# Optimization experiments

Hardware: AMD Instinct MI355X
Metric: run time of the kernel (lower is better)

## Reference

```python
import jax, jax.numpy as jnp
import numpy as np

B, S, D, H = 2, 2048, 1024, 16
DK = D // H

def setup_inputs() -> dict:
    key = jax.random.key(0)
    ks = jax.random.split(key, 12)
    sc = 0.02
    return {
        "q": jax.random.normal(ks[0], (B, S, D), jnp.float32),
        "k": jax.random.normal(ks[1], (B, S, D), jnp.float32),
        "v": jax.random.normal(ks[2], (B, S, D), jnp.float32),
        "mask": jnp.ones((1, 1, S, S), jnp.int32),
        "w_q": jax.random.normal(ks[3], (D, D), jnp.float32) * sc,
        "b_q": jnp.zeros((D,), jnp.float32),
        "w_k": jax.random.normal(ks[4], (D, D), jnp.float32) * sc,
        "b_k": jnp.zeros((D,), jnp.float32),
        "w_v": jax.random.normal(ks[5], (D, D), jnp.float32) * sc,
        "b_v": jnp.zeros((D,), jnp.float32),
        "w_o": jax.random.normal(ks[6], (D, D), jnp.float32) * sc,
        "b_o": jnp.zeros((D,), jnp.float32),
    }

def reference(q, k, v, mask, w_q, b_q, w_k, b_k, w_v, b_v, w_o, b_o):
    # torch Linear: y = x @ W.T + b, W is [out, in]
    def lin(x, w, b):
        return jnp.einsum('bsd,ed->bse', x, w) + b
    # project and split heads -> [B, H, S, DK]
    def heads(x):
        return x.reshape(B, S, H, DK).transpose(0, 2, 1, 3)
    Q = heads(lin(q, w_q, b_q))
    K = heads(lin(k, w_k, b_k))
    V = heads(lin(v, w_v, b_v))
    scores = jnp.einsum('bhqd,bhkd->bhqk', Q, K) / jnp.sqrt(jnp.float32(DK))
    scores = jnp.where(mask == 0, jnp.float32(-1e9), scores)
    attn = jax.nn.softmax(scores, axis=-1)  # dropout p=0 -> identity
    ctx = jnp.einsum('bhqk,bhkd->bhqd', attn, V)
    ctx = ctx.transpose(0, 2, 1, 3).reshape(B, S, D)
    return lin(ctx, w_o, b_o)
```

## Files before the change

### kernel.cpp

```cpp
#include <hip/hip_runtime.h>
#include <stdint.h>


#define S_LEN 2048
#define LOG2E 1.4426950408889634f

using bf16x8 = __attribute__((ext_vector_type(8))) __bf16;
using f32x4 = __attribute__((ext_vector_type(4))) float;
using f32x16 = __attribute__((ext_vector_type(16))) float;
using u32x4 = __attribute__((ext_vector_type(4))) unsigned int;

__device__ __forceinline__ unsigned short f2bf(float x) {
  unsigned int u = __builtin_bit_cast(unsigned int, x);
  u += 0x7fffu + ((u >> 16) & 1u);
  return (unsigned short)(u >> 16);
}

__device__ __forceinline__ void gload_lds16(const void* g, void* l) {
  __builtin_amdgcn_global_load_lds(
      (const __attribute__((address_space(1))) void*)g,
      (__attribute__((address_space(3))) void*)l, 16, 0, 0);
}

__device__ __forceinline__ unsigned int cvtpk(float lo, float hi) {
  unsigned int r;
  asm("v_cvt_pk_bf16_f32 %0, %1, %2" : "=v"(r) : "v"(lo), "v"(hi));
  return r;
}

__device__ __forceinline__ bf16x8 mkfrag(float p0, float p1, float p2, float p3,
                                         float p4, float p5, float p6, float p7) {
  auto r02 = __builtin_amdgcn_permlane32_swap(cvtpk(p0, p1), cvtpk(p4, p5),
                                              false, false);
  auto r13 = __builtin_amdgcn_permlane32_swap(cvtpk(p2, p3), cvtpk(p6, p7),
                                              false, false);
  u32x4 w = {(unsigned int)r02[0], (unsigned int)r13[0], (unsigned int)r02[1],
             (unsigned int)r13[1]};
  return __builtin_bit_cast(bf16x8, w);
}

__global__ void cvt4_kernel(const float* __restrict__ s0,
                            const float* __restrict__ s1,
                            const float* __restrict__ s2,
                            const float* __restrict__ s3,
                            unsigned short* __restrict__ d0,
                            unsigned short* __restrict__ d1,
                            unsigned short* __restrict__ d2,
                            unsigned short* __restrict__ d3, int n4) {
  const int which = blockIdx.y;
  const float* src = which == 0 ? s0 : which == 1 ? s1 : which == 2 ? s2 : s3;
  unsigned short* dst = which == 0 ? d0 : which == 1 ? d1 : which == 2 ? d2 : d3;
  int i = blockIdx.x * blockDim.x + threadIdx.x;
  int stride = gridDim.x * blockDim.x;
  for (; i < n4; i += stride) {
    float4 v = ((const float4*)src)[i];
    ushort4 o;
    o.x = f2bf(v.x);
    o.y = f2bf(v.y);
    o.z = f2bf(v.z);
    o.w = f2bf(v.w);
    ((ushort4*)dst)[i] = o;
  }
}

template <int OMODE>
__device__ __forceinline__ void qkv64_body(
    unsigned short* As, unsigned short* Bs, const float* __restrict__ X,
    const unsigned short* __restrict__ W, const float* __restrict__ bias,
    unsigned short* __restrict__ dst, float scale, int tx, int ty) {
  const int tid = threadIdx.x;
  const int wid = tid >> 6, lane = tid & 63;
  const int l15 = lane & 15, lg = lane >> 4;
  const int bm = ty * 64, bn = tx * 128;
  const int wr = (wid >> 1) * 32, wc = (wid & 1) * 64;

  const f32x4 fz = {0.f, 0.f, 0.f, 0.f};
  f32x4 acc[2][4];
#pragma unroll
  for (int m = 0; m < 2; ++m)
#pragma unroll
    for (int n = 0; n < 4; ++n) acc[m][n] = fz;

  const int ar = tid >> 2;
  const float* Af = X + (size_t)(bm + ar) * 1024 + (tid & 3) * 8;
  const int sA = (tid & 3) ^ ((tid >> 3) & 3);
  const int srow = lane >> 2;
  const int scolz = ((lane & 3) ^ ((lane >> 3) & 3)) * 8;
  const int rcol = (lg ^ ((l15 >> 1) & 3)) * 8;

  for (int kt = 0; kt < 1024; kt += 32) {
    float4 a0 = *(const float4*)(Af + kt);
    float4 a1 = *(const float4*)(Af + kt + 4);
#pragma unroll
    for (int c = 0; c < 2; ++c) {
      int ch = wid * 2 + c;
      gload_lds16(W + (size_t)(bn + ch * 16 + srow) * 1024 + kt + scolz,
                  Bs + ch * 512);
    }
    u32x4 p = {cvtpk(a0.x, a0.y), cvtpk(a0.z, a0.w), cvtpk(a1.x, a1.y),
               cvtpk(a1.z, a1.w)};
    *(u32x4*)&As[ar * 32 + sA * 8] = p;
    __syncthreads();

    bf16x8 af[2], bf[4];
#pragma unroll
    for (int m = 0; m < 2; ++m)
      af[m] = *(const bf16x8*)&As[(wr + m * 16 + l15) * 32 + rcol];
#pragma unroll
    for (int n = 0; n < 4; ++n)
      bf[n] = *(const bf16x8*)&Bs[(wc + n * 16 + l15) * 32 + rcol];

#pragma unroll
    for (int m = 0; m < 2; ++m)
#pragma unroll
      for (int n = 0; n < 4; ++n) {
        if (OMODE == 2)
          acc[m][n] = __builtin_amdgcn_mfma_f32_16x16x32_bf16(bf[n], af[m],
                                                              acc[m][n], 0, 0, 0);
        else
          acc[m][n] = __builtin_amdgcn_mfma_f32_16x16x32_bf16(af[m], bf[n],
                                                              acc[m][n], 0, 0, 0);
      }
    __syncthreads();
  }

#pragma unroll
  for (int m = 0; m < 2; ++m)
#pragma unroll
    for (int n = 0; n < 4; ++n)
#pragma unroll
      for (int j = 0; j < 4; ++j) {
        float a = acc[m][n][j];
        if (OMODE == 2) {
          int gn = bn + wc + n * 16 + lg * 4 + j;
          int gm = bm + wr + m * 16 + l15;
          float v = a + bias[gn];
          int b = gm >> 11, s = gm & 2047;
          int h = gn >> 6, dk = gn & 63;
          dst[(((size_t)(b * 16 + h)) * 64 + dk) * 2048 + s] = f2bf(v);
        } else {
          int gm = bm + wr + m * 16 + lg * 4 + j;
          int gn = bn + wc + n * 16 + l15;
          float v = (a + bias[gn]) * scale;
          int b = gm >> 11, s = gm & 2047;
          int h = gn >> 6, dk = gn & 63;
          dst[(((size_t)(b * 16 + h)) * 2048 + s) * 64 + dk] = f2bf(v);
        }
      }
}

__global__ __launch_bounds__(256) void gemm_qkv(
    const float* __restrict__ X0, const float* __restrict__ X1,
    const float* __restrict__ X2, const unsigned short* __restrict__ W0,
    const unsigned short* __restrict__ W1,
    const unsigned short* __restrict__ W2, const float* __restrict__ b0,
    const float* __restrict__ b1, const float* __restrict__ b2,
    unsigned short* __restrict__ dq, unsigned short* __restrict__ dk,
    unsigned short* __restrict__ dv) {
  __shared__ unsigned short As[64 * 32];
  __shared__ unsigned short Bs[128 * 32];
  const int lin = blockIdx.x + 8 * (blockIdx.y + 64 * blockIdx.z);
  const int xcd = lin & 7, v = lin >> 3;
  const int panel = xcd * 24 + (v >> 3);
  const int tx = v & 7;
  const int z = panel >> 6, ty = panel & 63;
  if (z == 0)
    qkv64_body<0>(As, Bs, X0, W0, b0, dq, 0.125f * LOG2E, tx, ty);
  else if (z == 1)
    qkv64_body<0>(As, Bs, X1, W1, b1, dk, 1.0f, tx, ty);
  else
    qkv64_body<2>(As, Bs, X2, W2, b2, dv, 1.0f, tx, ty);
}

__global__ __launch_bounds__(256) void gemm_out(
    const unsigned short* __restrict__ X, const unsigned short* __restrict__ W,
    const float* __restrict__ bias, float* __restrict__ dstF) {
  const int lin = blockIdx.x + 8 * blockIdx.y;
  const int xcd = lin & 7, v = lin >> 3;
  const int ty = xcd * 8 + (v >> 3);
  const int tx = v & 7;

  __shared__ unsigned short As[3][64 * 32];
  __shared__ unsigned short Bs[3][128 * 32];
  const int tid = threadIdx.x;
  const int wid = tid >> 6, lane = tid & 63;
  const int l15 = lane & 15, lg = lane >> 4;
  const int bm = ty * 64, bn = tx * 128;
  const int wr = (wid >> 1) * 32, wc = (wid & 1) * 64;

  const f32x4 fz = {0.f, 0.f, 0.f, 0.f};
  f32x4 acc[2][4];
#pragma unroll
  for (int m = 0; m < 2; ++m)
#pragma unroll
    for (int n = 0; n < 4; ++n) acc[m][n] = fz;

  const int srow = lane >> 2;
  const int scolz = ((lane & 3) ^ ((lane >> 3) & 3)) * 8;
  const int rcol = (lg ^ ((l15 >> 1) & 3)) * 8;

#define GSTAGE(buf, kt)                                                       \
  {                                                                           \
    gload_lds16(X + (size_t)(bm + wid * 16 + srow) * 1024 + (kt) + scolz,     \
                &As[buf][wid * 512]);                                         \
    _Pragma("unroll") for (int c = 0; c < 2; ++c) {                           \
      int ch = wid * 2 + c;                                                   \
      gload_lds16(W + (size_t)(bn + ch * 16 + srow) * 1024 + (kt) + scolz,    \
                  &Bs[buf][ch * 512]);                                        \
    }                                                                         \
  }

  GSTAGE(0, 0)
  GSTAGE(1, 32)
  int cur = 0;

  for (int it = 0; it < 32; ++it) {
    if (it < 31) {
      asm volatile("s_waitcnt vmcnt(3)\n\ts_barrier" ::: "memory");
    } else {
      asm volatile("s_waitcnt vmcnt(0)\n\ts_barrier" ::: "memory");
    }
    if (it < 30) {
      int nb = cur >= 1 ? cur - 1 : cur + 2;
      GSTAGE(nb, (it + 2) * 32)
    }

    bf16x8 af[2], bf[4];
#pragma unroll
    for (int m = 0; m < 2; ++m)
      af[m] = *(const bf16x8*)&As[cur][(wr + m * 16 + l15) * 32 + rcol];
#pragma unroll
    for (int n = 0; n < 4; ++n)
      bf[n] = *(const bf16x8*)&Bs[cur][(wc + n * 16 + l15) * 32 + rcol];

#pragma unroll
    for (int m = 0; m < 2; ++m)
#pragma unroll
      for (int n = 0; n < 4; ++n)
        acc[m][n] = __builtin_amdgcn_mfma_f32_16x16x32_bf16(af[m], bf[n],
                                                            acc[m][n], 0, 0, 0);
    cur = cur == 2 ? 0 : cur + 1;
  }
#undef GSTAGE

#pragma unroll
  for (int m = 0; m < 2; ++m)
#pragma unroll
    for (int n = 0; n < 4; ++n)
#pragma unroll
      for (int j = 0; j < 4; ++j) {
        int gm = bm + wr + m * 16 + lg * 4 + j;
        int gn = bn + wc + n * 16 + l15;
        dstF[(size_t)gm * 1024 + gn] = acc[m][n][j] + bias[gn];
      }
}

__global__ __launch_bounds__(256) void attn_kernel(
    const unsigned short* __restrict__ Q,
    const unsigned short* __restrict__ K,
    const unsigned short* __restrict__ VT,
    unsigned short* __restrict__ CTX) {
  const int orig = blockIdx.x;
  const int wg = (orig & 7) * 64 + (orig >> 3);
  const int bh = wg >> 4;
  const int qb = wg & 15;
  const int tid = threadIdx.x;
  const int w = tid >> 6;
  const int lane = tid & 63;
  const int l31 = lane & 31;
  const int hi = lane >> 5;
  const int q0 = qb * 128 + w * 32;

  __shared__ __align__(16) unsigned short Ks[3][64][64];
  __shared__ __align__(16) unsigned short Vs[3][64][64];
  __shared__ float ls[4][32];

  const unsigned short* Qg = Q + ((size_t)bh * S_LEN + q0) * 64;
  const unsigned short* Kg = K + (size_t)bh * S_LEN * 64;
  const unsigned short* Vg = VT + (size_t)bh * 64 * S_LEN;

  bf16x8 qf[4];
#pragma unroll
  for (int kc = 0; kc < 4; ++kc)
    qf[kc] = *(const bf16x8*)&Qg[l31 * 64 + kc * 16 + hi * 8];

  const int srow = lane >> 3;
  const int sslot = (lane & 7) ^ srow;

#define STAGE(buf, kt)                                                         \
  {                                                                            \
    gload_lds16(Kg + ((size_t)((kt) + w * 16 + srow)) * 64 + sslot * 8,        \
                &Ks[buf][w * 16][0]);                                          \
    gload_lds16(Kg + ((size_t)((kt) + w * 16 + 8 + srow)) * 64 + sslot * 8,    \
                &Ks[buf][w * 16 + 8][0]);                                      \
    gload_lds16(Vg + ((size_t)(w * 16 + srow)) * S_LEN + (kt) + sslot * 8,     \
                &Vs[buf][w * 16][0]);                                          \
    gload_lds16(Vg + ((size_t)(w * 16 + 8 + srow)) * S_LEN + (kt) + sslot * 8, \
                &Vs[buf][w * 16 + 8][0]);                                      \
  }

  f32x16 O0 = {}, O1 = {};
  float m = -1e30f, lsum = 0.f;

  STAGE(0, 0)
  STAGE(1, 64)
  int cur = 0;

  for (int t = 0; t < 32; ++t) {
    if (t < 31) {
      asm volatile("s_waitcnt vmcnt(4)\n\ts_barrier" ::: "memory");
    } else {
      asm volatile("s_waitcnt vmcnt(0)\n\ts_barrier" ::: "memory");
    }
    if (t < 30) {
      int nb = cur >= 1 ? cur - 1 : cur + 2;
      STAGE(nb, (t + 2) * 64)
    }

    f32x16 s0 = {}, s1 = {};
    __builtin_amdgcn_s_setprio(1);
#pragma unroll
    for (int kc = 0; kc < 4; ++kc) {
      const int col = ((kc * 2 + hi) ^ (l31 & 7)) * 8;
      bf16x8 kf0 = *(const bf16x8*)&Ks[cur][l31][col];
      bf16x8 kf1 = *(const bf16x8*)&Ks[cur][32 + l31][col];
      s0 = __builtin_amdgcn_mfma_f32_32x32x16_bf16(kf0, qf[kc], s0, 0, 0, 0);
      s1 = __builtin_amdgcn_mfma_f32_32x32x16_bf16(kf1, qf[kc], s1, 0, 0, 0);
    }
    __builtin_amdgcn_s_setprio(0);

    float tmax[8];
#pragma unroll
    for (int i = 0; i < 8; ++i)
      tmax[i] = fmaxf(fmaxf(s0[i], s0[i + 8]), fmaxf(s1[i], s1[i + 8]));
    float pm = fmaxf(fmaxf(fmaxf(tmax[0], tmax[1]), fmaxf(tmax[2], tmax[3])),
                     fmaxf(fmaxf(tmax[4], tmax[5]), fmaxf(tmax[6], tmax[7])));
    pm = fmaxf(pm, __shfl_xor(pm, 32, 64));

    if (!__all(pm - m <= 8.0f)) {
      float mn = fmaxf(m, pm);
      float al = exp2f(m - mn);
      m = mn;
      lsum *= al;
      ls[w][l31] = al;
#pragma unroll
      for (int r = 0; r < 16; ++r) {
        float a = ls[w][(r & 3) + 8 * (r >> 2) + 4 * hi];
        O0[r] *= a;
        O1[r] *= a;
      }
    }

#pragma unroll
    for (int r = 0; r < 16; ++r) {
      s0[r] = exp2f(s0[r] - m);
      s1[r] = exp2f(s1[r] - m);
    }
    float sa = 0.f, sb = 0.f, sc = 0.f, sd = 0.f;
#pragma unroll
    for (int r = 0; r < 4; ++r) {
      sa += s0[r];
      sb += s0[r + 4];
      sc += s0[r + 8];
      sd += s0[r + 12];
      sa += s1[r];
      sb += s1[r + 4];
      sc += s1[r + 8];
      sd += s1[r + 12];
    }
    float ts = (sa + sb) + (sc + sd);
    ts += __shfl_xor(ts, 32, 64);
    lsum += ts;

    bf16x8 pa0 = mkfrag(s0[0], s0[1], s0[2], s0[3], s0[4], s0[5], s0[6], s0[7]);
    bf16x8 pa1 =
        mkfrag(s0[8], s0[9], s0[10], s0[11], s0[12], s0[13], s0[14], s0[15]);
    bf16x8 pa2 = mkfrag(s1[0], s1[1], s1[2], s1[3], s1[4], s1[5], s1[6], s1[7]);
    bf16x8 pa3 =
        mkfrag(s1[8], s1[9], s1[10], s1[11], s1[12], s1[13], s1[14], s1[15]);

    __builtin_amdgcn_s_setprio(1);
#pragma unroll
    for (int kc = 0; kc < 4; ++kc) {
      const int col = ((kc * 2 + hi) ^ (l31 & 7)) * 8;
      bf16x8 v0 = *(const bf16x8*)&Vs[cur][l31][col];
      bf16x8 v1 = *(const bf16x8*)&Vs[cur][32 + l31][col];
      bf16x8 pa = (kc == 0) ? pa0 : (kc == 1) ? pa1 : (kc == 2) ? pa2 : pa3;
      O0 = __builtin_amdgcn_mfma_f32_32x32x16_bf16(pa, v0, O0, 0, 0, 0);
      O1 = __builtin_amdgcn_mfma_f32_32x32x16_bf16(pa, v1, O1, 0, 0, 0);
    }
    __builtin_amdgcn_s_setprio(0);

    cur = cur == 2 ? 0 : cur + 1;
  }

  ls[w][l31] = lsum;
  const int b = bh >> 4, h = bh & 15;
#pragma unroll
  for (int r = 0; r < 16; ++r) {
    int qr = (r & 3) + 8 * (r >> 2) + 4 * hi;
    float inv = __builtin_amdgcn_rcpf(ls[w][qr]);
    size_t base = ((size_t)b * S_LEN + q0 + qr) * 1024 + h * 64;
    CTX[base + l31] = f2bf(O0[r] * inv);
    CTX[base + 32 + l31] = f2bf(O1[r] * inv);
  }
#undef STAGE
}

extern "C" void kernel_launch(void* const* d_in, const int* in_sizes, int n_in,
                              void* d_out, int out_size, void* d_ws,
                              size_t ws_size, hipStream_t stream) {
  const float* q = (const float*)d_in[0];
  const float* k = (const float*)d_in[1];
  const float* v = (const float*)d_in[2];
  const float* wq = (const float*)d_in[4];
  const float* bq = (const float*)d_in[5];
  const float* wk = (const float*)d_in[6];
  const float* bk = (const float*)d_in[7];
  const float* wv = (const float*)d_in[8];
  const float* bv = (const float*)d_in[9];
  const float* wo = (const float*)d_in[10];
  const float* bo = (const float*)d_in[11];
  float* out = (float*)d_out;

  const size_t NTOK = 4096 * 1024;
  unsigned short* ws = (unsigned short*)d_ws;
  unsigned short* wqb = ws;
  unsigned short* wkb = wqb + 1048576;
  unsigned short* wvb = wkb + 1048576;
  unsigned short* wob = wvb + 1048576;
  unsigned short* Qp = wob + 1048576;
  unsigned short* Kp = Qp + NTOK;
  unsigned short* Vt = Kp + NTOK;
  unsigned short* CTX = Vt + NTOK;

  cvt4_kernel<<<dim3(256, 4), 256, 0, stream>>>(wq, wk, wv, wo, wqb, wkb, wvb,
                                                wob, 262144);

  gemm_qkv<<<dim3(8, 64, 3), 256, 0, stream>>>(q, k, v, wqb, wkb, wvb, bq, bk,
                                               bv, Qp, Kp, Vt);

  attn_kernel<<<512, 256, 0, stream>>>(Qp, Kp, Vt, CTX);

  gemm_out<<<dim3(8, 64), 256, 0, stream>>>(CTX, wob, bo, out);
}
```

Before: 149.4 us.

## Pre-convert activations, pipeline QKV GEMM, split attention KV into two halves

Measured after the change: 159.7 us. 1.07x slower.

```diff
diff --git a/kernel.cpp b/kernel.cpp
--- a/kernel.cpp
+++ b/kernel.cpp
@@ -14,6 +14,11 @@
   unsigned int u = __builtin_bit_cast(unsigned int, x);
   u += 0x7fffu + ((u >> 16) & 1u);
   return (unsigned short)(u >> 16);
+}
+
+__device__ __forceinline__ float bf2f(unsigned short u) {
+  unsigned int x = ((unsigned int)u) << 16;
+  return __builtin_bit_cast(float, x);
 }
 
 __device__ __forceinline__ void gload_lds16(const void* g, void* l) {
@@ -39,35 +44,53 @@
   return __builtin_bit_cast(bf16x8, w);
 }
 
-__global__ void cvt4_kernel(const float* __restrict__ s0,
-                            const float* __restrict__ s1,
-                            const float* __restrict__ s2,
-                            const float* __restrict__ s3,
-                            unsigned short* __restrict__ d0,
-                            unsigned short* __restrict__ d1,
-                            unsigned short* __restrict__ d2,
-                            unsigned short* __restrict__ d3, int n4) {
-  const int which = blockIdx.y;
-  const float* src = which == 0 ? s0 : which == 1 ? s1 : which == 2 ? s2 : s3;
-  unsigned short* dst = which == 0 ? d0 : which == 1 ? d1 : which == 2 ? d2 : d3;
+__global__ void cvt7_kernel(const float* __restrict__ q,
+                            const float* __restrict__ k,
+                            const float* __restrict__ v,
+                            const float* __restrict__ w0,
+                            const float* __restrict__ w1,
+                            const float* __restrict__ w2,
+                            const float* __restrict__ w3,
+                            unsigned short* __restrict__ dq,
+                            unsigned short* __restrict__ dk,
+                            unsigned short* __restrict__ dv,
+                            unsigned short* __restrict__ e0,
+                            unsigned short* __restrict__ e1,
+                            unsigned short* __restrict__ e2,
+                            unsigned short* __restrict__ e3) {
+  const int y = blockIdx.y;
+  const float* src;
+  unsigned short* dst;
+  int n4;
+  if (y < 3) {
+    src = y == 0 ? q : y == 1 ? k : v;
+    dst = y == 0 ? dq : y == 1 ? dk : dv;
+    n4 = 1048576;
+  } else {
+    int j = y - 3;
+    src = j == 0 ? w0 : j == 1 ? w1 : j == 2 ? w2 : w3;
+    dst = j == 0 ? e0 : j == 1 ? e1 : j == 2 ? e2 : e3;
+    n4 = 262144;
+  }
   int i = blockIdx.x * blockDim.x + threadIdx.x;
   int stride = gridDim.x * blockDim.x;
   for (; i < n4; i += stride) {
-    float4 v = ((const float4*)src)[i];
+    float4 a = ((const float4*)src)[i];
     ushort4 o;
-    o.x = f2bf(v.x);
-    o.y = f2bf(v.y);
-    o.z = f2bf(v.z);
-    o.w = f2bf(v.w);
+    o.x = f2bf(a.x);
+    o.y = f2bf(a.y);
+    o.z = f2bf(a.z);
+    o.w = f2bf(a.w);
     ((ushort4*)dst)[i] = o;
   }
 }
 
 template <int OMODE>
-__device__ __forceinline__ void qkv64_body(
-    unsigned short* As, unsigned short* Bs, const float* __restrict__ X,
-    const unsigned short* __restrict__ W, const float* __restrict__ bias,
-    unsigned short* __restrict__ dst, float scale, int tx, int ty) {
+__device__ __forceinline__ void gemm64_body(
+    unsigned short (*As)[2048], unsigned short (*Bs)[4096],
+    const unsigned short* __restrict__ X, const unsigned short* __restrict__ W,
+    const float* __restrict__ bias, unsigned short* __restrict__ dstB,
+    float* __restrict__ dstF, float scale, int tx, int ty) {
   const int tid = threadIdx.x;
   const int wid = tid >> 6, lane = tid & 63;
   const int l15 = lane & 15, lg = lane >> 4;
@@ -81,34 +104,43 @@
 #pragma unroll
     for (int n = 0; n < 4; ++n) acc[m][n] = fz;
 
-  const int ar = tid >> 2;
-  const float* Af = X + (size_t)(bm + ar) * 1024 + (tid & 3) * 8;
-  const int sA = (tid & 3) ^ ((tid >> 3) & 3);
   const int srow = lane >> 2;
   const int scolz = ((lane & 3) ^ ((lane >> 3) & 3)) * 8;
   const int rcol = (lg ^ ((l15 >> 1) & 3)) * 8;
 
-  for (int kt = 0; kt < 1024; kt += 32) {
-    float4 a0 = *(const float4*)(Af + kt);
-    float4 a1 = *(const float4*)(Af + kt + 4);
-#pragma unroll
-    for (int c = 0; c < 2; ++c) {
-      int ch = wid * 2 + c;
-      gload_lds16(W + (size_t)(bn + ch * 16 + srow) * 1024 + kt + scolz,
-                  Bs + ch * 512);
-    }
-    u32x4 p = {cvtpk(a0.x, a0.y), cvtpk(a0.z, a0.w), cvtpk(a1.x, a1.y),
-               cvtpk(a1.z, a1.w)};
-    *(u32x4*)&As[ar * 32 + sA * 8] = p;
-    __syncthreads();
+#define GS(buf, kt)                                                           \
+  {                                                                           \
+    gload_lds16(X + (size_t)(bm + wid * 16 + srow) * 1024 + (kt) + scolz,     \
+                &As[buf][wid * 512]);                                         \
+    _Pragma("unroll") for (int c = 0; c < 2; ++c) {                           \
+      int ch = wid * 2 + c;                                                   \
+      gload_lds16(W + (size_t)(bn + ch * 16 + srow) * 1024 + (kt) + scolz,    \
+                  &Bs[buf][ch * 512]);                                        \
+    }                                                                         \
+  }
+
+  GS(0, 0)
+  GS(1, 32)
+  int cur = 0;
+
+  for (int it = 0; it < 32; ++it) {
+    if (it < 31) {
+      asm volatile("s_waitcnt vmcnt(3)\n\ts_barrier" ::: "memory");
+    } else {
+      asm volatile("s_waitcnt vmcnt(0)\n\ts_barrier" ::: "memory");
+    }
+    if (it < 30) {
+      int nb = cur >= 1 ? cur - 1 : cur + 2;
+      GS(nb, (it + 2) * 32)
+    }
 
     bf16x8 af[2], bf[4];
 #pragma unroll
     for (int m = 0; m < 2; ++m)
-      af[m] = *(const bf16x8*)&As[(wr + m * 16 + l15) * 32 + rcol];
+      af[m] = *(const bf16x8*)&As[cur][(wr + m * 16 + l15) * 32 + rcol];
 #pragma unroll
     for (int n = 0; n < 4; ++n)
-      bf[n] = *(const bf16x8*)&Bs[(wc + n * 16 + l15) * 32 + rcol];
+      bf[n] = *(const bf16x8*)&Bs[cur][(wc + n * 16 + l15) * 32 + rcol];
 
 #pragma unroll
     for (int m = 0; m < 2; ++m)
@@ -121,8 +153,9 @@
           acc[m][n] = __builtin_amdgcn_mfma_f32_16x16x32_bf16(af[m], bf[n],
                                                               acc[m][n], 0, 0, 0);
       }
-    __syncthreads();
-  }
+    cur = cur == 2 ? 0 : cur + 1;
+  }
+#undef GS
 
 #pragma unroll
   for (int m = 0; m < 2; ++m)
@@ -131,139 +164,75 @@
 #pragma unroll
       for (int j = 0; j < 4; ++j) {
         float a = acc[m][n][j];
-        if (OMODE == 2) {
+        if (OMODE == 3) {
+          int gm = bm + wr + m * 16 + lg * 4 + j;
+          int gn = bn + wc + n * 16 + l15;
+          dstF[(size_t)gm * 1024 + gn] = a + bias[gn];
+        } else if (OMODE == 2) {
           int gn = bn + wc + n * 16 + lg * 4 + j;
           int gm = bm + wr + m * 16 + l15;
           float v = a + bias[gn];
           int b = gm >> 11, s = gm & 2047;
           int h = gn >> 6, dk = gn & 63;
-          dst[(((size_t)(b * 16 + h)) * 64 + dk) * 2048 + s] = f2bf(v);
+          dstB[(((size_t)(b * 16 + h)) * 64 + dk) * 2048 + s] = f2bf(v);
         } else {
           int gm = bm + wr + m * 16 + lg * 4 + j;
           int gn = bn + wc + n * 16 + l15;
           float v = (a + bias[gn]) * scale;
           int b = gm >> 11, s = gm & 2047;
           int h = gn >> 6, dk = gn & 63;
-          dst[(((size_t)(b * 16 + h)) * 2048 + s) * 64 + dk] = f2bf(v);
+          dstB[(((size_t)(b * 16 + h)) * 2048 + s) * 64 + dk] = f2bf(v);
         }
       }
 }
 
 __global__ __launch_bounds__(256) void gemm_qkv(
-    const float* __restrict__ X0, const float* __restrict__ X1,
-    const float* __restrict__ X2, const unsigned short* __restrict__ W0,
+    const unsigned short* __restrict__ X0, const unsigned short* __restrict__ X1,
+    const unsigned short* __restrict__ X2, const unsigned short* __restrict__ W0,
     const unsigned short* __restrict__ W1,
     const unsigned short* __restrict__ W2, const float* __restrict__ b0,
     const float* __restrict__ b1, const float* __restrict__ b2,
     unsigned short* __restrict__ dq, unsigned short* __restrict__ dk,
     unsigned short* __restrict__ dv) {
-  __shared__ unsigned short As[64 * 32];
-  __shared__ unsigned short Bs[128 * 32];
+  __shared__ unsigned short As[3][2048];
+  __shared__ unsigned short Bs[3][4096];
   const int lin = blockIdx.x + 8 * (blockIdx.y + 64 * blockIdx.z);
   const int xcd = lin & 7, v = lin >> 3;
   const int panel = xcd * 24 + (v >> 3);
   const int tx = v & 7;
   const int z = panel >> 6, ty = panel & 63;
   if (z == 0)
-    qkv64_body<0>(As, Bs, X0, W0, b0, dq, 0.125f * LOG2E, tx, ty);
+    gemm64_body<0>(As, Bs, X0, W0, b0, dq, nullptr, 0.125f * LOG2E, tx, ty);
   else if (z == 1)
-    qkv64_body<0>(As, Bs, X1, W1, b1, dk, 1.0f, tx, ty);
+    gemm64_body<0>(As, Bs, X1, W1, b1, dk, nullptr, 1.0f, tx, ty);
   else
-    qkv64_body<2>(As, Bs, X2, W2, b2, dv, 1.0f, tx, ty);
+    gemm64_body<2>(As, Bs, X2, W2, b2, dv, nullptr, 1.0f, tx, ty);
 }
 
 __global__ __launch_bounds__(256) void gemm_out(
     const unsigned short* __restrict__ X, const unsigned short* __restrict__ W,
     const float* __restrict__ bias, float* __restrict__ dstF) {
+  __shared__ unsigned short As[3][2048];
+  __shared__ unsigned short Bs[3][4096];
   const int lin = blockIdx.x + 8 * blockIdx.y;
   const int xcd = lin & 7, v = lin >> 3;
   const int ty = xcd * 8 + (v >> 3);
   const int tx = v & 7;
-
-  __shared__ unsigned short As[3][64 * 32];
-  __shared__ unsigned short Bs[3][128 * 32];
-  const int tid = threadIdx.x;
-  const int wid = tid >> 6, lane = tid & 63;
-  const int l15 = lane & 15, lg = lane >> 4;
-  const int bm = ty * 64, bn = tx * 128;
-  const int wr = (wid >> 1) * 32, wc = (wid & 1) * 64;
-
-  const f32x4 fz = {0.f, 0.f, 0.f, 0.f};
-  f32x4 acc[2][4];
-#pragma unroll
-  for (int m = 0; m < 2; ++m)
-#pragma unroll
-    for (int n = 0; n < 4; ++n) acc[m][n] = fz;
-
-  const int srow = lane >> 2;
-  const int scolz = ((lane & 3) ^ ((lane >> 3) & 3)) * 8;
-  const int rcol = (lg ^ ((l15 >> 1) & 3)) * 8;
-
-#define GSTAGE(buf, kt)                                                       \
-  {                                                                           \
-    gload_lds16(X + (size_t)(bm + wid * 16 + srow) * 1024 + (kt) + scolz,     \
-                &As[buf][wid * 512]);                                         \
-    _Pragma("unroll") for (int c = 0; c < 2; ++c) {                           \
-      int ch = wid * 2 + c;                                                   \
-      gload_lds16(W + (size_t)(bn + ch * 16 + srow) * 1024 + (kt) + scolz,    \
-                  &Bs[buf][ch * 512]);                                        \
-    }                                                                         \
-  }
-
-  GSTAGE(0, 0)
-  GSTAGE(1, 32)
-  int cur = 0;
-
-  for (int it = 0; it < 32; ++it) {
-    if (it < 31) {
-      asm volatile("s_waitcnt vmcnt(3)\n\ts_barrier" ::: "memory");
-    } else {
-      asm volatile("s_waitcnt vmcnt(0)\n\ts_barrier" ::: "memory");
-    }
-    if (it < 30) {
-      int nb = cur >= 1 ? cur - 1 : cur + 2;
-      GSTAGE(nb, (it + 2) * 32)
-    }
-
-    bf16x8 af[2], bf[4];
-#pragma unroll
-    for (int m = 0; m < 2; ++m)
-      af[m] = *(const bf16x8*)&As[cur][(wr + m * 16 + l15) * 32 + rcol];
-#pragma unroll
-    for (int n = 0; n < 4; ++n)
-      bf[n] = *(const bf16x8*)&Bs[cur][(wc + n * 16 + l15) * 32 + rcol];
-
-#pragma unroll
-    for (int m = 0; m < 2; ++m)
-#pragma unroll
-      for (int n = 0; n < 4; ++n)
-        acc[m][n] = __builtin_amdgcn_mfma_f32_16x16x32_bf16(af[m], bf[n],
-                                                            acc[m][n], 0, 0, 0);
-    cur = cur == 2 ? 0 : cur + 1;
-  }
-#undef GSTAGE
-
-#pragma unroll
-  for (int m = 0; m < 2; ++m)
-#pragma unroll
-    for (int n = 0; n < 4; ++n)
-#pragma unroll
-      for (int j = 0; j < 4; ++j) {
-        int gm = bm + wr + m * 16 + lg * 4 + j;
-        int gn = bn + wc + n * 16 + l15;
-        dstF[(size_t)gm * 1024 + gn] = acc[m][n][j] + bias[gn];
-      }
+  gemm64_body<3>(As, Bs, X, W, bias, nullptr, dstF, 1.0f, tx, ty);
 }
 
 __global__ __launch_bounds__(256) void attn_kernel(
     const unsigned short* __restrict__ Q,
     const unsigned short* __restrict__ K,
     const unsigned short* __restrict__ VT,
-    unsigned short* __restrict__ CTX) {
+    unsigned short* __restrict__ Opart, float2* __restrict__ ml) {
   const int orig = blockIdx.x;
-  const int wg = (orig & 7) * 64 + (orig >> 3);
-  const int bh = wg >> 4;
-  const int qb = wg & 15;
+  const int idx = (orig & 7) * 128 + (orig >> 3);
+  const int bh = idx >> 5;
+  const int u = idx & 31;
+  const int qb = u >> 1;
+  const int sp = u & 1;
+  const int kt0 = sp * 1024;
   const int tid = threadIdx.x;
   const int w = tid >> 6;
   const int lane = tid & 63;
@@ -271,8 +240,8 @@
   const int hi = lane >> 5;
   const int q0 = qb * 128 + w * 32;
 
-  __shared__ __align__(16) unsigned short Ks[3][64][64];
-  __shared__ __align__(16) unsigned short Vs[3][64][64];
+  __shared__ __align__(16) unsigned short Ks[2][64][64];
+  __shared__ __align__(16) unsigned short Vs[2][64][64];
   __shared__ float ls[4][32];
 
   const unsigned short* Qg = Q + ((size_t)bh * S_LEN + q0) * 64;
@@ -302,20 +271,12 @@
   f32x16 O0 = {}, O1 = {};
   float m = -1e30f, lsum = 0.f;
 
-  STAGE(0, 0)
-  STAGE(1, 64)
+  STAGE(0, kt0)
+  __syncthreads();
   int cur = 0;
 
-  for (int t = 0; t < 32; ++t) {
-    if (t < 31) {
-      asm volatile("s_waitcnt vmcnt(4)\n\ts_barrier" ::: "memory");
-    } else {
-      asm volatile("s_waitcnt vmcnt(0)\n\ts_barrier" ::: "memory");
-    }
-    if (t < 30) {
-      int nb = cur >= 1 ? cur - 1 : cur + 2;
-      STAGE(nb, (t + 2) * 64)
-    }
+  for (int t = 0; t < 16; ++t) {
+    if (t < 15) STAGE(cur ^ 1, kt0 + (t + 1) * 64)
 
     f32x16 s0 = {}, s1 = {};
     __builtin_amdgcn_s_setprio(1);
@@ -391,20 +352,60 @@
     }
     __builtin_amdgcn_s_setprio(0);
 
-    cur = cur == 2 ? 0 : cur + 1;
-  }
-
+    __syncthreads();
+    cur ^= 1;
+  }
+
+  if (hi == 0) {
+    float2 v2 = {m, lsum};
+    ml[(size_t)(sp * 32 + bh) * 2048 + q0 + l31] = v2;
+  }
   ls[w][l31] = lsum;
-  const int b = bh >> 4, h = bh & 15;
 #pragma unroll
   for (int r = 0; r < 16; ++r) {
     int qr = (r & 3) + 8 * (r >> 2) + 4 * hi;
     float inv = __builtin_amdgcn_rcpf(ls[w][qr]);
-    size_t base = ((size_t)b * S_LEN + q0 + qr) * 1024 + h * 64;
-    CTX[base + l31] = f2bf(O0[r] * inv);
-    CTX[base + 32 + l31] = f2bf(O1[r] * inv);
+    size_t base = ((size_t)(sp * 32 + bh) * 2048 + q0 + qr) * 64;
+    Opart[base + l31] = f2bf(O0[r] * inv);
+    Opart[base + 32 + l31] = f2bf(O1[r] * inv);
   }
 #undef STAGE
+}
+
+__global__ __launch_bounds__(256) void combine_kernel(
+    const unsigned short* __restrict__ Op, const float2* __restrict__ ml,
+    unsigned short* __restrict__ CTX) {
+  const int idx = blockIdx.x * 256 + threadIdx.x;
+  const int row = idx >> 3;
+  const int d0 = (idx & 7) * 8;
+  const float2 m1 = ml[row];
+  const float2 m2 = ml[65536 + row];
+  const float M = fmaxf(m1.x, m2.x);
+  const float a1 = exp2f(m1.x - M) * m1.y;
+  const float a2 = exp2f(m2.x - M) * m2.y;
+  const float inv = 1.0f / (a1 + a2);
+  const float w1 = a1 * inv, w2 = a2 * inv;
+  const size_t SPLIT = (size_t)32 * 2048 * 64;
+  ushort4 v1a = *(const ushort4*)&Op[(size_t)row * 64 + d0];
+  ushort4 v1b = *(const ushort4*)&Op[(size_t)row * 64 + d0 + 4];
+  ushort4 v2a = *(const ushort4*)&Op[SPLIT + (size_t)row * 64 + d0];
+  ushort4 v2b = *(const ushort4*)&Op[SPLIT + (size_t)row * 64 + d0 + 4];
+  unsigned short o8[8];
+  const unsigned short* p1 = (const unsigned short*)&v1a;
+  const unsigned short* p2 = (const unsigned short*)&v2a;
+  ushort4 vv1[2] = {v1a, v1b};
+  ushort4 vv2[2] = {v2a, v2b};
+  const unsigned short* q1 = (const unsigned short*)vv1;
+  const unsigned short* q2 = (const unsigned short*)vv2;
+#pragma unroll
+  for (int j = 0; j < 8; ++j)
+    o8[j] = f2bf(w1 * bf2f(q1[j]) + w2 * bf2f(q2[j]));
+  const int bh = row >> 11, s = row & 2047;
+  const int b = bh >> 4, h = bh & 15;
+  size_t o = ((size_t)(b * 2048 + s)) * 1024 + h * 64 + d0;
+  *(u32x4*)&CTX[o] = *(const u32x4*)o8;
+  (void)p1;
+  (void)p2;
 }
 
 extern "C" void kernel_launch(void* const* d_in, const int* in_sizes, int n_in,
@@ -425,22 +426,29 @@
 
   const size_t NTOK = 4096 * 1024;
   unsigned short* ws = (unsigned short*)d_ws;
-  unsigned short* wqb = ws;
+  unsigned short* xq = ws;
+  unsigned short* xk = xq + NTOK;
+  unsigned short* xv = xk + NTOK;
+  unsigned short* wqb = xv + NTOK;
   unsigned short* wkb = wqb + 1048576;
   unsigned short* wvb = wkb + 1048576;
   unsigned short* wob = wvb + 1048576;
   unsigned short* Qp = wob + 1048576;
   unsigned short* Kp = Qp + NTOK;
   unsigned short* Vt = Kp + NTOK;
-  unsigned short* CTX = Vt + NTOK;
-
-  cvt4_kernel<<<dim3(256, 4), 256, 0, stream>>>(wq, wk, wv, wo, wqb, wkb, wvb,
-                                                wob, 262144);
-
-  gemm_qkv<<<dim3(8, 64, 3), 256, 0, stream>>>(q, k, v, wqb, wkb, wvb, bq, bk,
-                                               bv, Qp, Kp, Vt);
-
-  attn_kernel<<<512, 256, 0, stream>>>(Qp, Kp, Vt, CTX);
+  unsigned short* Opart = ws;
+  float2* ml = (float2*)(ws + 8388608);
+  unsigned short* CTX = Qp;
+
+  cvt7_kernel<<<dim3(512, 7), 256, 0, stream>>>(q, k, v, wq, wk, wv, wo, xq, xk,
+                                                xv, wqb, wkb, wvb, wob);
+
+  gemm_qkv<<<dim3(8, 64, 3), 256, 0, stream>>>(xq, xk, xv, wqb, wkb, wvb, bq,
+                                               bk, bv, Qp, Kp, Vt);
+
+  attn_kernel<<<1024, 256, 0, stream>>>(Qp, Kp, Vt, Opart, ml);
+
+  combine_kernel<<<2048, 256, 0, stream>>>(Opart, ml, CTX);
 
   gemm_out<<<dim3(8, 64), 256, 0, stream>>>(CTX, wob, bo, out);
 }
```
